# Kernel tuning notes

Measured on AMD Instinct MI355X. Metric: run time of the kernel, lower is better.

## Reference

```python
import jax, jax.numpy as jnp
import numpy as np

N_NODES = 100000
N_EDGES = 1600000
N_GRAPHS = 100
HEADS = 8
OUT_CH = 16
IN_FEAT = 128
EPS = 1e-5
NEG_SLOPE = 0.2


def setup_inputs() -> dict:
    key = jax.random.key(0)
    ks = jax.random.split(key, 8)
    x = jax.random.normal(ks[0], (N_NODES, IN_FEAT), dtype=jnp.float32)
    edge_index = jax.random.randint(ks[1], (2, N_EDGES), 0, N_NODES, dtype=jnp.int64)
    batch = jnp.sort(jax.random.randint(ks[2], (N_NODES,), 0, N_GRAPHS, dtype=jnp.int64))
    bn_gamma = jnp.ones((IN_FEAT,), jnp.float32)
    bn_beta = jnp.zeros((IN_FEAT,), jnp.float32)
    W = jax.random.normal(ks[3], (IN_FEAT, HEADS * OUT_CH), dtype=jnp.float32) * (1.0 / np.sqrt(IN_FEAT))
    att_src = jax.random.normal(ks[4], (HEADS, OUT_CH), dtype=jnp.float32) * 0.1
    att_dst = jax.random.normal(ks[5], (HEADS, OUT_CH), dtype=jnp.float32) * 0.1
    bias = jnp.zeros((OUT_CH,), jnp.float32)
    return {"x": x, "edge_index": edge_index, "batch": batch,
            "bn_gamma": bn_gamma, "bn_beta": bn_beta, "W": W,
            "att_src": att_src, "att_dst": att_dst, "bias": bias}


def reference(x, edge_index, batch, bn_gamma, bn_beta, W, att_src, att_dst, bias):
    N = x.shape[0]
    # BatchNorm1d (training mode: batch statistics, biased variance)
    mean = jnp.mean(x, axis=0)
    var = jnp.var(x, axis=0)
    xn = (x - mean) * jax.lax.rsqrt(var + EPS) * bn_gamma + bn_beta

    # GATConv (heads=HEADS, concat=False), with self-loops as in PyG default
    loop = jnp.arange(N, dtype=edge_index.dtype)
    src = jnp.concatenate([edge_index[0], loop])  # [Et]
    dst = jnp.concatenate([edge_index[1], loop])  # [Et]

    h = (xn @ W).reshape(N, HEADS, OUT_CH)  # [N,H,C]
    a_src = jnp.einsum('nhc,hc->nh', h, att_src)  # [N,H]
    a_dst = jnp.einsum('nhc,hc->nh', h, att_dst)  # [N,H]

    e = a_src[src] + a_dst[dst]  # [Et,H]
    e = jnp.where(e > 0, e, NEG_SLOPE * e)  # leaky_relu(0.2)
    # scatter-softmax over destination node (self-loops => every segment nonempty)
    m = jax.ops.segment_max(e, dst, num_segments=N)  # [N,H]
    e = jnp.exp(e - m[dst])
    s = jax.ops.segment_sum(e, dst, num_segments=N)  # [N,H]
    alpha = e / s[dst]  # [Et,H]

    msg = alpha[:, :, None] * h[src]  # [Et,H,C]
    out = jax.ops.segment_sum(msg, dst, num_segments=N)  # [N,H,C]
    out = out.mean(axis=1) + bias  # concat=False -> head mean, [N,C]

    out = jax.nn.elu(out)

    # global_mean_pool over graph ids
    sums = jax.ops.segment_sum(out, batch, num_segments=N_GRAPHS)  # [G,C]
    cnt = jax.ops.segment_sum(jnp.ones((N,), out.dtype), batch, num_segments=N_GRAPHS)
    return sums / jnp.maximum(cnt, 1.0)[:, None]
```

## Files before the change

kernel.cpp:

```cpp
#include <hip/hip_runtime.h>
#include <hip/hip_bf16.h>
#include <hip/hip_fp16.h>


#define N_NODES 100000
#define N_EDGE  1600000
#define N_ET    1700000
#define N_G     100
#define HEADS   8
#define OUTC    16
#define EPS     1e-5f
#define NEG     0.2f
#define NB_BUCKETS 391
#define BCAP    4864
#define BNB     384
#define ABB     640
#define EPB     2657
#define ESLOTS  11

typedef unsigned int uint;
typedef unsigned short ushort;
typedef float f32x2 __attribute__((ext_vector_type(2)));
typedef float f32x4 __attribute__((ext_vector_type(4)));
typedef __bf16 bf16x8 __attribute__((ext_vector_type(8)));

__device__ __forceinline__ float bf2f_lo(uint u){ union{uint i; float f;} c; c.i = u << 16; return c.f; }
__device__ __forceinline__ float bf2f_hi(uint u){ union{uint i; float f;} c; c.i = u & 0xffff0000u; return c.f; }
__device__ __forceinline__ float bf2f(ushort u){ union{uint i; float f;} c; c.i = ((uint)u) << 16; return c.f; }
__device__ __forceinline__ float scrub(float v){ return (v == v) ? v : 0.f; }

__device__ __forceinline__ ushort f2bf(float f){
  union{float ff; uint u;} c; c.ff = f;
  uint u = c.u;
  if ((u & 0x7fffffffu) > 0x7f800000u) u = 0;
  return (ushort)((u + 0x7fffu + ((u >> 16) & 1u)) >> 16);
}
__device__ __forceinline__ ushort bfsan(ushort u){
  return ((ushort)(u & 0x7fffu) > (ushort)0x7f80u) ? (ushort)0 : u;
}

__device__ __forceinline__ float ldf(const void* p, int i, int f32){
  return f32 ? ((const float*)p)[i] : bf2f(((const ushort*)p)[i]);
}
__device__ __forceinline__ int ldid(const int* p, int flat, int is64){
  return is64 ? p[2 * flat] : p[flat];
}

__global__ __launch_bounds__(256) void k_front(const void* __restrict__ xraw,
                                               float* __restrict__ stats,
                                               const int* __restrict__ ei,
                                               int* __restrict__ bcnt,
                                               uint* __restrict__ pairBuf){
  int t = threadIdx.x;
  if (blockIdx.x < BNB){
    __shared__ int cdet;
    __shared__ float red[4][256];
    if (t == 0) cdet = 0;
    __syncthreads();
    { uint w = ((const uint*)xraw)[t]; uint el = (w >> 7) & 0xffu;
      if (el != 0 && (el < 110 || el > 140)) atomicAdd(&cdet, 1); }
    __syncthreads();
    int f32 = cdet > 64;
    int c = t & 63;
    int c0 = c * 2;
    float s0 = 0.f, s1 = 0.f, q0 = 0.f, q1 = 0.f;
    if (f32){
      const float2* x2 = (const float2*)xraw;
      for (int r = blockIdx.x * 4 + (t >> 6); r < N_NODES; r += BNB * 4){
        float2 v = x2[r * 64 + c];
        float f0 = scrub(v.x), f1 = scrub(v.y);
        s0 += f0; q0 += f0 * f0;
        s1 += f1; q1 += f1 * f1;
      }
    } else {
      const uint* x2 = (const uint*)xraw;
      for (int r = blockIdx.x * 4 + (t >> 6); r < N_NODES; r += BNB * 4){
        uint v = x2[r * 64 + c];
        float f0 = scrub(bf2f_lo(v)), f1 = scrub(bf2f_hi(v));
        s0 += f0; q0 += f0 * f0;
        s1 += f1; q1 += f1 * f1;
      }
    }
    red[0][t] = s0; red[1][t] = q0; red[2][t] = s1; red[3][t] = q1;
    __syncthreads();
    if (t < 64){
      s0 = red[0][t] + red[0][t+64] + red[0][t+128] + red[0][t+192];
      q0 = red[1][t] + red[1][t+64] + red[1][t+128] + red[1][t+192];
      s1 = red[2][t] + red[2][t+64] + red[2][t+128] + red[2][t+192];
      q1 = red[3][t] + red[3][t+64] + red[3][t+128] + red[3][t+192];
      atomicAdd(&stats[c0],       s0);
      atomicAdd(&stats[c0+1],     s1);
      atomicAdd(&stats[128+c0],   q0);
      atomicAdd(&stats[128+c0+1], q1);
    }
  } else {
    __shared__ int hist[NB_BUCKETS];
    __shared__ int base[NB_BUCKETS];
    __shared__ int cdet2;
    int bid = blockIdx.x - BNB;
    if (t == 0) cdet2 = 0;
    for (int i = t; i < NB_BUCKETS; i += 256) hist[i] = 0;
    __syncthreads();
    if (t < 128){ if (ei[2 * t + 1] != 0) atomicAdd(&cdet2, 1); }
    __syncthreads();
    int is64 = cdet2 < 32;
    int e0 = bid * EPB, e1 = min(e0 + EPB, N_ET);
    uint preg[ESLOTS];
    int  breg[ESLOTS];
#pragma unroll
    for (int j = 0; j < ESLOTS; j++){
      int e = e0 + t + j * 256;
      uint pk = 0; int b = -1;
      if (e < e1){
        int s, d;
        if (e < N_EDGE){ s = ldid(ei, e, is64); d = ldid(ei, N_EDGE + e, is64); }
        else { s = d = e - N_EDGE; }
        uint dd = (uint)d; if (dd >= N_NODES) dd = 0;
        uint ss = (uint)s; if (ss >= N_NODES) ss = 0;
        b = (int)(dd >> 8);
        pk = (ss << 8) | (dd & 255u);
        atomicAdd(&hist[b], 1);
      }
      preg[j] = pk; breg[j] = b;
    }
    __syncthreads();
    for (int i = t; i < NB_BUCKETS; i += 256){
      int c = hist[i];
      base[i] = c ? atomicAdd(&bcnt[i], c) : 0;
      hist[i] = 0;
    }
    __syncthreads();
#pragma unroll
    for (int j = 0; j < ESLOTS; j++){
      int b = breg[j];
      if (b >= 0){
        int pos = base[b] + atomicAdd(&hist[b], 1);
        if ((uint)pos < BCAP) pairBuf[(size_t)b * BCAP + pos] = preg[j];
      }
    }
  }
}

__global__ __launch_bounds__(512) void k_mid(const float* __restrict__ stats,
                                             const void* __restrict__ gamma,
                                             const void* __restrict__ beta,
                                             const void* __restrict__ W,
                                             const uint* __restrict__ x32,
                                             const int* __restrict__ b32,
                                             ushort* __restrict__ Wpb,
                                             float* __restrict__ bp,
                                             int* __restrict__ flags,
                                             const uint* __restrict__ pairBuf,
                                             const int* __restrict__ bcnt,
                                             int* __restrict__ offsets,
                                             int* __restrict__ csr){
  int t = threadIdx.x;
  if (blockIdx.x < 16){
    __shared__ int cnt2[2];
    __shared__ float scl8[8], shf8[8];
    int bid = blockIdx.x;
    if (t < 2) cnt2[t] = 0;
    __syncthreads();
    if (t < 128){
      { uint w = x32[t];       uint el = (w >> 7) & 0xffu;
        if (el != 0 && (el < 110 || el > 140)) atomicAdd(&cnt2[0], 1); }
      { uint w = x32[t + 128]; uint el = (w >> 7) & 0xffu;
        if (el != 0 && (el < 110 || el > 140)) atomicAdd(&cnt2[0], 1); }
      if (bid == 0){ if (b32[98001 + 2 * t] != 0) atomicAdd(&cnt2[1], 1); }
    }
    __syncthreads();
    int f32 = cnt2[0] > 64;
    if (bid == 0 && t == 0){
      flags[0] = f32;
      flags[1] = 0;
      flags[2] = cnt2[1] < 32;
      flags[3] = 0;
    }
    if (t < 8){
      int c = bid * 8 + t;
      float mean = scrub(stats[c] * (1.0f / N_NODES));
      float var  = stats[128 + c] * (1.0f / N_NODES) - mean * mean;
      if (!(var > 0.f)) var = 0.f;
      float sc = scrub(ldf(gamma, c, f32)) * rsqrtf(var + EPS);
      sc = scrub(sc);
      scl8[t] = sc;
      shf8[t] = scrub(scrub(ldf(beta, c, f32)) - mean * sc);
    }
    __syncthreads();
    if (t < 128){
      float bacc = 0.f;
#pragma unroll
      for (int j = 0; j < 8; j++){
        int c = bid * 8 + j;
        float w = scrub(ldf(W, c * 128 + t, f32));
        Wpb[t * 128 + (c & 7) + (((c >> 3) ^ (t & 15)) << 3)] = f2bf(scl8[j] * w);
        bacc += shf8[j] * w;
      }
      atomicAdd(&bp[t], scrub(bacc));
    }
  } else {
    __shared__ int sscan[512];
    __shared__ int degL[256];
    __shared__ int offL[256];
    __shared__ int curL[256];
    int b = blockIdx.x - 16;
    sscan[t] = (t < NB_BUCKETS) ? min(bcnt[t], BCAP) : 0;
    if (t < 256) degL[t] = 0;
    __syncthreads();
    for (int off = 1; off < 512; off <<= 1){
      int add = (t >= off) ? sscan[t - off] : 0;
      __syncthreads();
      sscan[t] += add;
      __syncthreads();
    }
    int gbase = (b == 0) ? 0 : sscan[b - 1];
    if (b == NB_BUCKETS - 1 && t == 0) offsets[N_NODES] = sscan[NB_BUCKETS - 1];
    int cnt = min(bcnt[b], BCAP);
    const uint* run = pairBuf + (size_t)b * BCAP;
    for (int i = t; i < cnt; i += 512)
      atomicAdd(&degL[run[i] & 255u], 1);
    __syncthreads();
    int v = (t < 256) ? degL[t] : 0;
    if (t < 256) offL[t] = v;
    __syncthreads();
    for (int off = 1; off < 256; off <<= 1){
      int add = (t < 256 && t >= off) ? offL[t - off] : 0;
      __syncthreads();
      if (t < 256) offL[t] += add;
      __syncthreads();
    }
    if (t < 256){
      int excl = offL[t] - v;
      int node = (b << 8) + t;
      if (node < N_NODES) offsets[node] = gbase + excl;
      offL[t] = excl;
      curL[t] = 0;
    }
    __syncthreads();
    for (int i = t; i < cnt; i += 512){
      uint e = run[i];
      int dl = e & 255u;
      int s  = e >> 8;
      int pos = atomicAdd(&curL[dl], 1);
      csr[gbase + offL[dl] + pos] = s;
    }
  }
}

__global__ __launch_bounds__(256) void k_gemm(const void* __restrict__ xraw,
                                              const ushort* __restrict__ Wpb,
                                              const float* __restrict__ bp,
                                              const void* __restrict__ att_src,
                                              const void* __restrict__ att_dst,
                                              const int* __restrict__ flags,
                                              unsigned char* __restrict__ h8,
                                              __half* __restrict__ a_src16,
                                              __half* __restrict__ a_dst16){
  int f32 = flags[0];
  __shared__ __align__(16) char smem[33792];
  __shared__ float sSL[128], sDL[128], bpL[128];
  int t = threadIdx.x;
  int wv = t >> 6, l = t & 63;
  int row0 = blockIdx.x * 64;
  if (t < 128){
    sSL[t] = scrub(ldf(att_src, t, f32));
    sDL[t] = scrub(ldf(att_dst, t, f32));
    bpL[t] = bp[t];
  }
  {
    const uint4* wsrc = (const uint4*)Wpb;
    uint4* wdst = (uint4*)smem;
#pragma unroll
    for (int i = 0; i < 8; i++)
      wdst[i * 256 + t] = wsrc[i * 256 + t];
  }
  __syncthreads();
  ushort* BsT = (ushort*)smem;

  f32x4 acc[8];
#pragma unroll
  for (int ct = 0; ct < 8; ct++) acc[ct] = (f32x4){0.f, 0.f, 0.f, 0.f};
  int arow = row0 + wv * 16 + (l & 15);
  int cr = min(arow, N_NODES - 1);
  int kg = (l >> 4) * 8;
  union AB { uint4 q; bf16x8 v; ushort u[8]; };
#pragma unroll
  for (int kc = 0; kc < 4; kc++){
    AB a;
    if (f32){
      const float* xr = (const float*)xraw + (size_t)cr * 128 + kc * 32 + kg;
      float4 p0 = *(const float4*)xr;
      float4 p1 = *(const float4*)(xr + 4);
      a.u[0] = f2bf(p0.x); a.u[1] = f2bf(p0.y); a.u[2] = f2bf(p0.z); a.u[3] = f2bf(p0.w);
      a.u[4] = f2bf(p1.x); a.u[5] = f2bf(p1.y); a.u[6] = f2bf(p1.z); a.u[7] = f2bf(p1.w);
    } else {
      const ushort* xr = (const ushort*)xraw + (size_t)cr * 128 + kc * 32 + kg;
      a.q = *(const uint4*)xr;
#pragma unroll
      for (int j = 0; j < 8; j++) a.u[j] = bfsan(a.u[j]);
    }
#pragma unroll
    for (int ct = 0; ct < 8; ct++){
      int c = ct * 16 + (l & 15);
      int kb = kc * 4 + (l >> 4);
      AB bfr;
      bfr.q = *(const uint4*)(BsT + c * 128 + ((kb ^ (c & 15)) << 3));
      acc[ct] = __builtin_amdgcn_mfma_f32_16x16x32_bf16(a.v, bfr.v, acc[ct], 0, 0, 0);
    }
  }
  __syncthreads();
  float* Cs = (float*)smem;
#pragma unroll
  for (int ct = 0; ct < 8; ct++){
#pragma unroll
    for (int ri = 0; ri < 4; ri++)
      Cs[(wv * 16 + (l >> 4) * 4 + ri) * 132 + ct * 16 + (l & 15)] = acc[ct][ri];
  }
  __syncthreads();
  int row = t >> 2, cg = (t & 3) * 32;
  int r = row0 + row;
  if (r < N_NODES){
    float o[32];
#pragma unroll
    for (int i = 0; i < 8; i++){
      float4 v = *(const float4*)(Cs + row * 132 + cg + i * 4);
      o[i*4+0] = v.x; o[i*4+1] = v.y; o[i*4+2] = v.z; o[i*4+3] = v.w;
    }
#pragma unroll
    for (int j = 0; j < 32; j++){
      float v = scrub(o[j] + bpL[cg + j]);
      o[j] = fminf(fmaxf(v, -448.f), 448.f);
    }
    uint w[8];
#pragma unroll
    for (int i = 0; i < 8; i++){
      uint ww = __builtin_amdgcn_cvt_pk_fp8_f32(o[i*4+0], o[i*4+1], 0, false);
      w[i] = __builtin_amdgcn_cvt_pk_fp8_f32(o[i*4+2], o[i*4+3], (int)ww, true);
    }
    unsigned char* po = h8 + (size_t)r * 128 + cg;
    *(uint4*)po        = make_uint4(w[0], w[1], w[2], w[3]);
    *(uint4*)(po + 16) = make_uint4(w[4], w[5], w[6], w[7]);
    float s0 = 0.f, s1 = 0.f, d0 = 0.f, d1 = 0.f;
#pragma unroll
    for (int j = 0; j < 16; j++){
      s0 += o[j]      * sSL[cg + j];      d0 += o[j]      * sDL[cg + j];
      s1 += o[16 + j] * sSL[cg + 16 + j]; d1 += o[16 + j] * sDL[cg + 16 + j];
    }
    int hA = (t & 3) * 2;
    *(__half2*)(a_src16 + (size_t)r * 8 + hA) = __floats2half2_rn(scrub(s0), scrub(s1));
    *(__half2*)(a_dst16 + (size_t)r * 8 + hA) = __floats2half2_rn(scrub(d0), scrub(d1));
  }
}

__global__ __launch_bounds__(256) void k_msg(const int* __restrict__ offsets, const int* __restrict__ csr,
                                             const __half* __restrict__ a_src16, const __half* __restrict__ a_dst16,
                                             const uint* __restrict__ h32, const void* __restrict__ bias,
                                             const int* __restrict__ flags,
                                             float* __restrict__ out_n){
  int f32 = flags[0];
  int t = threadIdx.x;
  int wv = t >> 6, lane = t & 63;
  int half = lane >> 5, li = lane & 31;
  int myh = li >> 2;
  int n = blockIdx.x * 4 + wv;
  int start = offsets[n], end = offsets[n + 1];
  float ad = __half2float(a_dst16[(size_t)n * 8 + myh]);
  const ushort* as16 = (const ushort*)a_src16;
  float acc0 = 0.f, acc1 = 0.f, acc2 = 0.f, acc3 = 0.f, den = 0.f;

#define PAIR(AA, HH)                                                  \
  { float e = __half2float(*(__half*)&(AA)) + ad;                     \
    e = fmaxf(e, NEG * e);                                            \
    float p = __expf(fminf(e, 30.f));                                 \
    f32x2 lo = __builtin_amdgcn_cvt_pk_f32_fp8((int)(HH), false);     \
    f32x2 hi = __builtin_amdgcn_cvt_pk_f32_fp8((int)(HH), true);      \
    den += p; acc0 += p * lo[0]; acc1 += p * lo[1];                   \
    acc2 += p * hi[0]; acc3 += p * hi[1]; }

  for (int base = start; base < end; base += 64){
    int cnt = min(64, end - base);
    int sreg = csr[min(base + lane, N_ET - 1)];
    int npair = cnt >> 1;
    int jj = 0;
    for (; jj + 4 <= npair; jj += 4){
      int i0 = 2 * jj + half;
      int s0 = __shfl(sreg, i0);
      int s1 = __shfl(sreg, i0 + 2);
      int s2 = __shfl(sreg, i0 + 4);
      int s3 = __shfl(sreg, i0 + 6);
      uint h0 = h32[(uint)s0 * 32u + li];
      uint h1 = h32[(uint)s1 * 32u + li];
      uint h2 = h32[(uint)s2 * 32u + li];
      uint h3 = h32[(uint)s3 * 32u + li];
      ushort a0 = as16[(uint)s0 * 8u + myh];
      ushort a1 = as16[(uint)s1 * 8u + myh];
      ushort a2 = as16[(uint)s2 * 8u + myh];
      ushort a3 = as16[(uint)s3 * 8u + myh];
      __builtin_amdgcn_sched_barrier(0);
      PAIR(a0, h0) PAIR(a1, h1) PAIR(a2, h2) PAIR(a3, h3)
    }
    for (; jj < npair; jj++){
      int s0 = __shfl(sreg, 2 * jj + half);
      uint h0 = h32[(uint)s0 * 32u + li];
      ushort a0 = as16[(uint)s0 * 8u + myh];
      PAIR(a0, h0)
    }
    if (cnt & 1){
      int sl = __shfl(sreg, cnt - 1);
      uint hh = h32[(uint)sl * 32u + li];
      ushort aa = as16[(uint)sl * 8u + myh];
      float e = __half2float(*(__half*)&aa) + ad;
      e = fmaxf(e, NEG * e);
      float p = __expf(fminf(e, 30.f));
      p = half ? 0.f : p;
      f32x2 lo = __builtin_amdgcn_cvt_pk_f32_fp8((int)hh, false);
      f32x2 hi = __builtin_amdgcn_cvt_pk_f32_fp8((int)hh, true);
      den += p; acc0 += p * lo[0]; acc1 += p * lo[1];
      acc2 += p * hi[0]; acc3 += p * hi[1];
    }
  }
#undef PAIR

  den  += __shfl_xor(den, 32);
  acc0 += __shfl_xor(acc0, 32);
  acc1 += __shfl_xor(acc1, 32);
  acc2 += __shfl_xor(acc2, 32);
  acc3 += __shfl_xor(acc3, 32);
  float inv = (den > 0.f) ? (1.0f / den) : 0.f;
  float v0 = acc0 * inv, v1 = acc1 * inv, v2 = acc2 * inv, v3 = acc3 * inv;
  v0 += __shfl_xor(v0, 4);  v1 += __shfl_xor(v1, 4);  v2 += __shfl_xor(v2, 4);  v3 += __shfl_xor(v3, 4);
  v0 += __shfl_xor(v0, 8);  v1 += __shfl_xor(v1, 8);  v2 += __shfl_xor(v2, 8);  v3 += __shfl_xor(v3, 8);
  v0 += __shfl_xor(v0, 16); v1 += __shfl_xor(v1, 16); v2 += __shfl_xor(v2, 16); v3 += __shfl_xor(v3, 16);
  if (lane < 4){
    int c0 = lane * 4;
    float o0 = v0 * 0.125f + scrub(ldf(bias, c0 + 0, f32));
    float o1 = v1 * 0.125f + scrub(ldf(bias, c0 + 1, f32));
    float o2 = v2 * 0.125f + scrub(ldf(bias, c0 + 2, f32));
    float o3 = v3 * 0.125f + scrub(ldf(bias, c0 + 3, f32));
    o0 = o0 > 0.f ? o0 : (__expf(o0) - 1.0f);
    o1 = o1 > 0.f ? o1 : (__expf(o1) - 1.0f);
    o2 = o2 > 0.f ? o2 : (__expf(o2) - 1.0f);
    o3 = o3 > 0.f ? o3 : (__expf(o3) - 1.0f);
    float4* po = (float4*)(out_n + (size_t)n * 16 + c0);
    *po = make_float4(scrub(o0), scrub(o1), scrub(o2), scrub(o3));
  }
}

__global__ __launch_bounds__(256) void k_pool(const float* __restrict__ out_n,
                                              const int* __restrict__ batch,
                                              const int* __restrict__ flags,
                                              float* __restrict__ out){
  int b64 = flags[2];
  int g = blockIdx.x;
  int t = threadIdx.x;
  int c = t & 15, rg = t >> 4;
  int lo = 0, hi = N_NODES;
  while (lo < hi){ int m = (lo + hi) >> 1; if (ldid(batch, m, b64) < g) lo = m + 1; else hi = m; }
  int lo2 = lo, hi2 = N_NODES;
  while (lo2 < hi2){ int m = (lo2 + hi2) >> 1; if (ldid(batch, m, b64) < g + 1) lo2 = m + 1; else hi2 = m; }
  float acc = 0.f;
  for (int r = lo + rg; r < lo2; r += 16)
    acc += out_n[(size_t)r * 16 + c];
  __shared__ float red[16][17];
  red[rg][c] = acc;
  __syncthreads();
  if (t < 16){
    float v = 0.f;
#pragma unroll
    for (int i = 0; i < 16; i++) v += red[i][t];
    float cntf = (float)(lo2 - lo);
    out[g * 16 + t] = scrub(v / fmaxf(cntf, 1.0f));
  }
}

extern "C" void kernel_launch(void* const* d_in, const int* in_sizes, int n_in,
                              void* d_out, int out_size, void* d_ws, size_t ws_size,
                              hipStream_t stream){
  (void)in_sizes; (void)n_in; (void)out_size; (void)ws_size;
  const void* x     = d_in[0];
  const int*  ei    = (const int*)d_in[1];
  const int*  batch = (const int*)d_in[2];
  const void* gamma = d_in[3];
  const void* beta  = d_in[4];
  const void* W     = d_in[5];
  const void* att_s = d_in[6];
  const void* att_d = d_in[7];
  const void* bias  = d_in[8];

  char* ws = (char*)d_ws;
  size_t off = 0;
  auto alloc = [&](size_t b){ size_t r = off; off += (b + 255) & ~(size_t)255; return r; };
  int*    flags   = (int*)(ws + alloc(4 * 4));
  float*  stats   = (float*)(ws + alloc(256 * 4));
  float*  bp      = (float*)(ws + alloc(128 * 4));
  int*    bcnt    = (int*)(ws + alloc(NB_BUCKETS * 4));
  size_t  zero_end = off;
  ushort* Wpb     = (ushort*)(ws + alloc(16384 * 2));
  int*    offsets = (int*)(ws + alloc((size_t)(N_NODES + 1) * 4));
  __half* a_src16 = (__half*)(ws + alloc((size_t)N_NODES * 8 * 2));
  __half* a_dst16 = (__half*)(ws + alloc((size_t)N_NODES * 8 * 2));
  size_t  pb_bytes = (size_t)NB_BUCKETS * BCAP * 4;
  size_t  on_bytes = (size_t)N_NODES * 16 * 4;
  char*   pb_region = ws + alloc(pb_bytes > on_bytes ? pb_bytes : on_bytes);
  uint*   pairBuf = (uint*)pb_region;
  float*  out_n   = (float*)pb_region;
  unsigned char* h8 = (unsigned char*)(ws + alloc((size_t)N_NODES * 128));
  int*    csr     = (int*)(ws + alloc((size_t)N_ET * 4));

  hipMemsetAsync(ws, 0, zero_end, stream);

  k_front<<<BNB + ABB, 256, 0, stream>>>(x, stats, ei, bcnt, pairBuf);
  k_mid<<<16 + NB_BUCKETS, 512, 0, stream>>>(stats, gamma, beta, W, (const uint*)x, batch,
                                             Wpb, bp, flags, pairBuf, bcnt, offsets, csr);
  k_gemm<<<(N_NODES + 63) / 64, 256, 0, stream>>>(x, Wpb, bp, att_s, att_d, flags, h8, a_src16, a_dst16);
  k_msg<<<N_NODES / 4, 256, 0, stream>>>(offsets, csr, a_src16, a_dst16, (const uint*)h8, bias, flags, out_n);
  k_pool<<<N_G, 256, 0, stream>>>(out_n, batch, flags, (float*)d_out);
}
```

Baseline: 274.8 us.

## Split BN/W prep into tiny kernel and co-schedule CSR build with GEMM

The weight-folding and flag computation moves into a small 16-block kernel. The CSR bucket-scatter work moves out of the mid kernel and into the GEMM launch as extra blocks, so CSR construction runs alongside the GEMM tiles instead of in its own launch. The CSR path now uses 256 threads per block with a two-element scan. This trades one kernel boundary for a heterogeneous launch whose CSR blocks share the GEMM's larger shared-memory footprint, which may lower their occupancy.

```diff
diff --git a/kernel.cpp b/kernel.cpp
--- a/kernel.cpp
+++ b/kernel.cpp
@@ -17,6 +17,7 @@
 #define ABB     640
 #define EPB     2657
 #define ESLOTS  11
+#define GEMMB   1563
 
 typedef unsigned int uint;
 typedef unsigned short ushort;
@@ -141,214 +142,208 @@
   }
 }
 
-__global__ __launch_bounds__(512) void k_mid(const float* __restrict__ stats,
-                                             const void* __restrict__ gamma,
-                                             const void* __restrict__ beta,
-                                             const void* __restrict__ W,
-                                             const uint* __restrict__ x32,
-                                             const int* __restrict__ b32,
-                                             ushort* __restrict__ Wpb,
-                                             float* __restrict__ bp,
-                                             int* __restrict__ flags,
-                                             const uint* __restrict__ pairBuf,
-                                             const int* __restrict__ bcnt,
-                                             int* __restrict__ offsets,
-                                             int* __restrict__ csr){
+__global__ __launch_bounds__(128) void k_prep(const float* __restrict__ stats,
+                                              const void* __restrict__ gamma,
+                                              const void* __restrict__ beta,
+                                              const void* __restrict__ W,
+                                              const uint* __restrict__ x32,
+                                              const int* __restrict__ b32,
+                                              ushort* __restrict__ Wpb,
+                                              float* __restrict__ bp,
+                                              int* __restrict__ flags){
+  __shared__ int cnt[2];
+  __shared__ float scl8[8], shf8[8];
+  int t = threadIdx.x, bid = blockIdx.x;
+  if (t < 2) cnt[t] = 0;
+  __syncthreads();
+  { uint w = x32[t];       uint el = (w >> 7) & 0xffu;
+    if (el != 0 && (el < 110 || el > 140)) atomicAdd(&cnt[0], 1); }
+  { uint w = x32[t + 128]; uint el = (w >> 7) & 0xffu;
+    if (el != 0 && (el < 110 || el > 140)) atomicAdd(&cnt[0], 1); }
+  if (bid == 0){ if (b32[98001 + 2 * t] != 0) atomicAdd(&cnt[1], 1); }
+  __syncthreads();
+  int f32 = cnt[0] > 64;
+  if (bid == 0 && t == 0){
+    flags[0] = f32;
+    flags[1] = 0;
+    flags[2] = cnt[1] < 32;
+    flags[3] = 0;
+  }
+  if (t < 8){
+    int c = bid * 8 + t;
+    float mean = scrub(stats[c] * (1.0f / N_NODES));
+    float var  = stats[128 + c] * (1.0f / N_NODES) - mean * mean;
+    if (!(var > 0.f)) var = 0.f;
+    float sc = scrub(ldf(gamma, c, f32)) * rsqrtf(var + EPS);
+    sc = scrub(sc);
+    scl8[t] = sc;
+    shf8[t] = scrub(scrub(ldf(beta, c, f32)) - mean * sc);
+  }
+  __syncthreads();
+  float bacc = 0.f;
+#pragma unroll
+  for (int j = 0; j < 8; j++){
+    int c = bid * 8 + j;
+    float w = scrub(ldf(W, c * 128 + t, f32));
+    Wpb[t * 128 + (c & 7) + (((c >> 3) ^ (t & 15)) << 3)] = f2bf(scl8[j] * w);
+    bacc += shf8[j] * w;
+  }
+  atomicAdd(&bp[t], scrub(bacc));
+}
+
+__global__ __launch_bounds__(256) void k_gemmC(const void* __restrict__ xraw,
+                                               const ushort* __restrict__ Wpb,
+                                               const float* __restrict__ bp,
+                                               const void* __restrict__ att_src,
+                                               const void* __restrict__ att_dst,
+                                               const int* __restrict__ flags,
+                                               unsigned char* __restrict__ h8,
+                                               __half* __restrict__ a_src16,
+                                               __half* __restrict__ a_dst16,
+                                               const uint* __restrict__ pairBuf,
+                                               const int* __restrict__ bcnt,
+                                               int* __restrict__ offsets,
+                                               int* __restrict__ csr){
+  __shared__ __align__(16) char smem[33792];
+  __shared__ float sSL[128], sDL[128], bpL[128];
   int t = threadIdx.x;
-  if (blockIdx.x < 16){
-    __shared__ int cnt2[2];
-    __shared__ float scl8[8], shf8[8];
-    int bid = blockIdx.x;
-    if (t < 2) cnt2[t] = 0;
-    __syncthreads();
-    if (t < 128){
-      { uint w = x32[t];       uint el = (w >> 7) & 0xffu;
-        if (el != 0 && (el < 110 || el > 140)) atomicAdd(&cnt2[0], 1); }
-      { uint w = x32[t + 128]; uint el = (w >> 7) & 0xffu;
-        if (el != 0 && (el < 110 || el > 140)) atomicAdd(&cnt2[0], 1); }
-      if (bid == 0){ if (b32[98001 + 2 * t] != 0) atomicAdd(&cnt2[1], 1); }
-    }
-    __syncthreads();
-    int f32 = cnt2[0] > 64;
-    if (bid == 0 && t == 0){
-      flags[0] = f32;
-      flags[1] = 0;
-      flags[2] = cnt2[1] < 32;
-      flags[3] = 0;
-    }
-    if (t < 8){
-      int c = bid * 8 + t;
-      float mean = scrub(stats[c] * (1.0f / N_NODES));
-      float var  = stats[128 + c] * (1.0f / N_NODES) - mean * mean;
-      if (!(var > 0.f)) var = 0.f;
-      float sc = scrub(ldf(gamma, c, f32)) * rsqrtf(var + EPS);
-      sc = scrub(sc);
-      scl8[t] = sc;
-      shf8[t] = scrub(scrub(ldf(beta, c, f32)) - mean * sc);
-    }
-    __syncthreads();
-    if (t < 128){
-      float bacc = 0.f;
-#pragma unroll
-      for (int j = 0; j < 8; j++){
-        int c = bid * 8 + j;
-        float w = scrub(ldf(W, c * 128 + t, f32));
-        Wpb[t * 128 + (c & 7) + (((c >> 3) ^ (t & 15)) << 3)] = f2bf(scl8[j] * w);
-        bacc += shf8[j] * w;
-      }
-      atomicAdd(&bp[t], scrub(bacc));
-    }
-  } else {
-    __shared__ int sscan[512];
-    __shared__ int degL[256];
-    __shared__ int offL[256];
-    __shared__ int curL[256];
-    int b = blockIdx.x - 16;
-    sscan[t] = (t < NB_BUCKETS) ? min(bcnt[t], BCAP) : 0;
-    if (t < 256) degL[t] = 0;
+  if (blockIdx.x < NB_BUCKETS){
+    int* sscan = (int*)smem;
+    int* degL  = (int*)(smem + 2048);
+    int* offL  = (int*)(smem + 3072);
+    int* curL  = (int*)(smem + 4096);
+    int b = blockIdx.x;
+    sscan[t]       = (t < NB_BUCKETS) ? min(bcnt[t], BCAP) : 0;
+    sscan[t + 256] = (t + 256 < NB_BUCKETS) ? min(bcnt[t + 256], BCAP) : 0;
+    degL[t] = 0;
     __syncthreads();
     for (int off = 1; off < 512; off <<= 1){
-      int add = (t >= off) ? sscan[t - off] : 0;
+      int a0 = (t >= off) ? sscan[t - off] : 0;
+      int a1 = (t + 256 >= off) ? sscan[t + 256 - off] : 0;
       __syncthreads();
-      sscan[t] += add;
+      sscan[t] += a0; sscan[t + 256] += a1;
       __syncthreads();
     }
     int gbase = (b == 0) ? 0 : sscan[b - 1];
     if (b == NB_BUCKETS - 1 && t == 0) offsets[N_NODES] = sscan[NB_BUCKETS - 1];
     int cnt = min(bcnt[b], BCAP);
     const uint* run = pairBuf + (size_t)b * BCAP;
-    for (int i = t; i < cnt; i += 512)
+    for (int i = t; i < cnt; i += 256)
       atomicAdd(&degL[run[i] & 255u], 1);
     __syncthreads();
-    int v = (t < 256) ? degL[t] : 0;
-    if (t < 256) offL[t] = v;
+    int v = degL[t];
+    offL[t] = v;
     __syncthreads();
     for (int off = 1; off < 256; off <<= 1){
-      int add = (t < 256 && t >= off) ? offL[t - off] : 0;
+      int add = (t >= off) ? offL[t - off] : 0;
       __syncthreads();
-      if (t < 256) offL[t] += add;
+      offL[t] += add;
       __syncthreads();
     }
-    if (t < 256){
-      int excl = offL[t] - v;
-      int node = (b << 8) + t;
-      if (node < N_NODES) offsets[node] = gbase + excl;
-      offL[t] = excl;
-      curL[t] = 0;
-    }
-    __syncthreads();
-    for (int i = t; i < cnt; i += 512){
+    int excl = offL[t] - v;
+    int node = (b << 8) + t;
+    if (node < N_NODES) offsets[node] = gbase + excl;
+    offL[t] = excl;
+    curL[t] = 0;
+    __syncthreads();
+    for (int i = t; i < cnt; i += 256){
       uint e = run[i];
       int dl = e & 255u;
-      int s  = e >> 8;
       int pos = atomicAdd(&curL[dl], 1);
-      csr[gbase + offL[dl] + pos] = s;
-    }
-  }
-}
-
-__global__ __launch_bounds__(256) void k_gemm(const void* __restrict__ xraw,
-                                              const ushort* __restrict__ Wpb,
-                                              const float* __restrict__ bp,
-                                              const void* __restrict__ att_src,
-                                              const void* __restrict__ att_dst,
-                                              const int* __restrict__ flags,
-                                              unsigned char* __restrict__ h8,
-                                              __half* __restrict__ a_src16,
-                                              __half* __restrict__ a_dst16){
-  int f32 = flags[0];
-  __shared__ __align__(16) char smem[33792];
-  __shared__ float sSL[128], sDL[128], bpL[128];
-  int t = threadIdx.x;
-  int wv = t >> 6, l = t & 63;
-  int row0 = blockIdx.x * 64;
-  if (t < 128){
-    sSL[t] = scrub(ldf(att_src, t, f32));
-    sDL[t] = scrub(ldf(att_dst, t, f32));
-    bpL[t] = bp[t];
-  }
-  {
-    const uint4* wsrc = (const uint4*)Wpb;
-    uint4* wdst = (uint4*)smem;
-#pragma unroll
-    for (int i = 0; i < 8; i++)
-      wdst[i * 256 + t] = wsrc[i * 256 + t];
-  }
-  __syncthreads();
-  ushort* BsT = (ushort*)smem;
-
-  f32x4 acc[8];
-#pragma unroll
-  for (int ct = 0; ct < 8; ct++) acc[ct] = (f32x4){0.f, 0.f, 0.f, 0.f};
-  int arow = row0 + wv * 16 + (l & 15);
-  int cr = min(arow, N_NODES - 1);
-  int kg = (l >> 4) * 8;
-  union AB { uint4 q; bf16x8 v; ushort u[8]; };
-#pragma unroll
-  for (int kc = 0; kc < 4; kc++){
-    AB a;
-    if (f32){
-      const float* xr = (const float*)xraw + (size_t)cr * 128 + kc * 32 + kg;
-      float4 p0 = *(const float4*)xr;
-      float4 p1 = *(const float4*)(xr + 4);
-      a.u[0] = f2bf(p0.x); a.u[1] = f2bf(p0.y); a.u[2] = f2bf(p0.z); a.u[3] = f2bf(p0.w);
-      a.u[4] = f2bf(p1.x); a.u[5] = f2bf(p1.y); a.u[6] = f2bf(p1.z); a.u[7] = f2bf(p1.w);
-    } else {
-      const ushort* xr = (const ushort*)xraw + (size_t)cr * 128 + kc * 32 + kg;
-      a.q = *(const uint4*)xr;
-#pragma unroll
-      for (int j = 0; j < 8; j++) a.u[j] = bfsan(a.u[j]);
-    }
+      csr[gbase + offL[dl] + pos] = (int)(e >> 8);
+    }
+  } else {
+    int f32 = flags[0];
+    int wv = t >> 6, l = t & 63;
+    int row0 = (blockIdx.x - NB_BUCKETS) * 64;
+    if (t < 128){
+      sSL[t] = scrub(ldf(att_src, t, f32));
+      sDL[t] = scrub(ldf(att_dst, t, f32));
+      bpL[t] = bp[t];
+    }
+    {
+      const uint4* wsrc = (const uint4*)Wpb;
+      uint4* wdst = (uint4*)smem;
+#pragma unroll
+      for (int i = 0; i < 8; i++)
+        wdst[i * 256 + t] = wsrc[i * 256 + t];
+    }
+    __syncthreads();
+    ushort* BsT = (ushort*)smem;
+
+    f32x4 acc[8];
+#pragma unroll
+    for (int ct = 0; ct < 8; ct++) acc[ct] = (f32x4){0.f, 0.f, 0.f, 0.f};
+    int arow = row0 + wv * 16 + (l & 15);
+    int cr = min(arow, N_NODES - 1);
+    int kg = (l >> 4) * 8;
+    union AB { uint4 q; bf16x8 v; ushort u[8]; };
+#pragma unroll
+    for (int kc = 0; kc < 4; kc++){
+      AB a;
+      if (f32){
+        const float* xr = (const float*)xraw + (size_t)cr * 128 + kc * 32 + kg;
+        float4 p0 = *(const float4*)xr;
+        float4 p1 = *(const float4*)(xr + 4);
+        a.u[0] = f2bf(p0.x); a.u[1] = f2bf(p0.y); a.u[2] = f2bf(p0.z); a.u[3] = f2bf(p0.w);
+        a.u[4] = f2bf(p1.x); a.u[5] = f2bf(p1.y); a.u[6] = f2bf(p1.z); a.u[7] = f2bf(p1.w);
+      } else {
+        const ushort* xr = (const ushort*)xraw + (size_t)cr * 128 + kc * 32 + kg;
+        a.q = *(const uint4*)xr;
+#pragma unroll
+        for (int j = 0; j < 8; j++) a.u[j] = bfsan(a.u[j]);
+      }
+#pragma unroll
+      for (int ct = 0; ct < 8; ct++){
+        int c = ct * 16 + (l & 15);
+        int kb = kc * 4 + (l >> 4);
+        AB bfr;
+        bfr.q = *(const uint4*)(BsT + c * 128 + ((kb ^ (c & 15)) << 3));
+        acc[ct] = __builtin_amdgcn_mfma_f32_16x16x32_bf16(a.v, bfr.v, acc[ct], 0, 0, 0);
+      }
+    }
+    __syncthreads();
+    float* Cs = (float*)smem;
 #pragma unroll
     for (int ct = 0; ct < 8; ct++){
-      int c = ct * 16 + (l & 15);
-      int kb = kc * 4 + (l >> 4);
-      AB bfr;
-      bfr.q = *(const uint4*)(BsT + c * 128 + ((kb ^ (c & 15)) << 3));
-      acc[ct] = __builtin_amdgcn_mfma_f32_16x16x32_bf16(a.v, bfr.v, acc[ct], 0, 0, 0);
-    }
-  }
-  __syncthreads();
-  float* Cs = (float*)smem;
-#pragma unroll
-  for (int ct = 0; ct < 8; ct++){
-#pragma unroll
-    for (int ri = 0; ri < 4; ri++)
-      Cs[(wv * 16 + (l >> 4) * 4 + ri) * 132 + ct * 16 + (l & 15)] = acc[ct][ri];
-  }
-  __syncthreads();
-  int row = t >> 2, cg = (t & 3) * 32;
-  int r = row0 + row;
-  if (r < N_NODES){
-    float o[32];
-#pragma unroll
-    for (int i = 0; i < 8; i++){
-      float4 v = *(const float4*)(Cs + row * 132 + cg + i * 4);
-      o[i*4+0] = v.x; o[i*4+1] = v.y; o[i*4+2] = v.z; o[i*4+3] = v.w;
-    }
-#pragma unroll
-    for (int j = 0; j < 32; j++){
-      float v = scrub(o[j] + bpL[cg + j]);
-      o[j] = fminf(fmaxf(v, -448.f), 448.f);
-    }
-    uint w[8];
-#pragma unroll
-    for (int i = 0; i < 8; i++){
-      uint ww = __builtin_amdgcn_cvt_pk_fp8_f32(o[i*4+0], o[i*4+1], 0, false);
-      w[i] = __builtin_amdgcn_cvt_pk_fp8_f32(o[i*4+2], o[i*4+3], (int)ww, true);
-    }
-    unsigned char* po = h8 + (size_t)r * 128 + cg;
-    *(uint4*)po        = make_uint4(w[0], w[1], w[2], w[3]);
-    *(uint4*)(po + 16) = make_uint4(w[4], w[5], w[6], w[7]);
-    float s0 = 0.f, s1 = 0.f, d0 = 0.f, d1 = 0.f;
-#pragma unroll
-    for (int j = 0; j < 16; j++){
-      s0 += o[j]      * sSL[cg + j];      d0 += o[j]      * sDL[cg + j];
-      s1 += o[16 + j] * sSL[cg + 16 + j]; d1 += o[16 + j] * sDL[cg + 16 + j];
-    }
-    int hA = (t & 3) * 2;
-    *(__half2*)(a_src16 + (size_t)r * 8 + hA) = __floats2half2_rn(scrub(s0), scrub(s1));
-    *(__half2*)(a_dst16 + (size_t)r * 8 + hA) = __floats2half2_rn(scrub(d0), scrub(d1));
+#pragma unroll
+      for (int ri = 0; ri < 4; ri++)
+        Cs[(wv * 16 + (l >> 4) * 4 + ri) * 132 + ct * 16 + (l & 15)] = acc[ct][ri];
+    }
+    __syncthreads();
+    int row = t >> 2, cg = (t & 3) * 32;
+    int r = row0 + row;
+    if (r < N_NODES){
+      float o[32];
+#pragma unroll
+      for (int i = 0; i < 8; i++){
+        float4 v = *(const float4*)(Cs + row * 132 + cg + i * 4);
+        o[i*4+0] = v.x; o[i*4+1] = v.y; o[i*4+2] = v.z; o[i*4+3] = v.w;
+      }
+#pragma unroll
+      for (int j = 0; j < 32; j++){
+        float v = scrub(o[j] + bpL[cg + j]);
+        o[j] = fminf(fmaxf(v, -448.f), 448.f);
+      }
+      uint w[8];
+#pragma unroll
+      for (int i = 0; i < 8; i++){
+        uint ww = __builtin_amdgcn_cvt_pk_fp8_f32(o[i*4+0], o[i*4+1], 0, false);
+        w[i] = __builtin_amdgcn_cvt_pk_fp8_f32(o[i*4+2], o[i*4+3], (int)ww, true);
+      }
+      unsigned char* po = h8 + (size_t)r * 128 + cg;
+      *(uint4*)po        = make_uint4(w[0], w[1], w[2], w[3]);
+      *(uint4*)(po + 16) = make_uint4(w[4], w[5], w[6], w[7]);
+      float s0 = 0.f, s1 = 0.f, d0 = 0.f, d1 = 0.f;
+#pragma unroll
+      for (int j = 0; j < 16; j++){
+        s0 += o[j]      * sSL[cg + j];      d0 += o[j]      * sDL[cg + j];
+        s1 += o[16 + j] * sSL[cg + 16 + j]; d1 += o[16 + j] * sDL[cg + 16 + j];
+      }
+      int hA = (t & 3) * 2;
+      *(__half2*)(a_src16 + (size_t)r * 8 + hA) = __floats2half2_rn(scrub(s0), scrub(s1));
+      *(__half2*)(a_dst16 + (size_t)r * 8 + hA) = __floats2half2_rn(scrub(d0), scrub(d1));
+    }
   }
 }
 
@@ -510,9 +505,10 @@
   hipMemsetAsync(ws, 0, zero_end, stream);
 
   k_front<<<BNB + ABB, 256, 0, stream>>>(x, stats, ei, bcnt, pairBuf);
-  k_mid<<<16 + NB_BUCKETS, 512, 0, stream>>>(stats, gamma, beta, W, (const uint*)x, batch,
-                                             Wpb, bp, flags, pairBuf, bcnt, offsets, csr);
-  k_gemm<<<(N_NODES + 63) / 64, 256, 0, stream>>>(x, Wpb, bp, att_s, att_d, flags, h8, a_src16, a_dst16);
+  k_prep<<<16, 128, 0, stream>>>(stats, gamma, beta, W, (const uint*)x, batch, Wpb, bp, flags);
+  k_gemmC<<<NB_BUCKETS + GEMMB, 256, 0, stream>>>(x, Wpb, bp, att_s, att_d, flags,
+                                                  h8, a_src16, a_dst16,
+                                                  pairBuf, bcnt, offsets, csr);
   k_msg<<<N_NODES / 4, 256, 0, stream>>>(offsets, csr, a_src16, a_dst16, (const uint*)h8, bias, flags, out_n);
   k_pool<<<N_G, 256, 0, stream>>>(out_n, batch, flags, (float*)d_out);
 }
```

New measurement: 274.3 us. No clear change (-0.2%).
